# Optimization experiments

Measured on AMD Instinct MI355X. Metric: run time of the kernel, lower is better.

The kernel has to match this reference:

```python
import jax, jax.numpy as jnp
import numpy as np

N_EMBED = 1024
HEAD_SIZE = 128
B, T = 8, 2048


def setup_inputs() -> dict:
    key = jax.random.key(0)
    kx, kk, kq, kv = jax.random.split(key, 4)
    x = jax.random.normal(kx, (B, T, N_EMBED), dtype=jnp.float32)
    Wk = jax.random.normal(kk, (N_EMBED, HEAD_SIZE), dtype=jnp.float32) * (N_EMBED ** -0.5)
    Wq = jax.random.normal(kq, (N_EMBED, HEAD_SIZE), dtype=jnp.float32) * (N_EMBED ** -0.5)
    Wv = jax.random.normal(kv, (N_EMBED, HEAD_SIZE), dtype=jnp.float32) * (N_EMBED ** -0.5)
    return {"x": x, "Wk": Wk, "Wq": Wq, "Wv": Wv}


def reference(x, Wk, Wq, Wv):
    # x: [B, T, C]; single-head causal attention, dropout rate 0 (identity)
    t = x.shape[1]
    k = jnp.einsum("btc,ch->bth", x, Wk)  # keys
    q = jnp.einsum("btc,ch->bth", x, Wq)  # queries
    v = jnp.einsum("btc,ch->bth", x, Wv)  # values
    scale = k.shape[-1] ** -0.5
    scores = jnp.einsum("bqh,bkh->bqk", q, k) * scale  # [B, T, T]
    causal = jnp.tril(jnp.ones((t, t), dtype=bool))
    scores = jnp.where(causal, scores, -jnp.inf)
    attn = jax.nn.softmax(scores, axis=-1)
    return jnp.einsum("bqk,bkh->bqh", attn, v)
```

## Files before the change

### kernel.cpp

```cpp
#include <hip/hip_runtime.h>
#include <hip/hip_bf16.h>
#include <math.h>

#define B_ 8
#define T_ 2048
#define C_ 1024
#define D_ 128
#define M_ (B_*T_)

typedef __attribute__((ext_vector_type(8))) short short8;
typedef __attribute__((ext_vector_type(4))) float floatx4;
typedef __hip_bfloat16 bf16;

#define QSCALE 0.12751744416218247f

__global__ __launch_bounds__(256) void cvt_w3_kernel(const float* __restrict__ Wq,
                                                     const float* __restrict__ Wk,
                                                     const float* __restrict__ Wv,
                                                     bf16* __restrict__ Wt2) {
    __shared__ bf16 tl[64][136];
    const int t = threadIdx.x;
    const int kc = blockIdx.x, g = blockIdx.y;
    const int k0 = kc * 64;
    const float* W = (g == 0) ? Wq : (g == 1) ? Wk : Wv;
    {
        int k = t >> 2, n0 = (t & 3) * 32;
        const float* src = W + (size_t)(k0 + k) * 128 + n0;
#pragma unroll
        for (int j = 0; j < 4; ++j) {
            float4 v0 = *(const float4*)(src + j * 8);
            float4 v1 = *(const float4*)(src + j * 8 + 4);
            union { short8 s; __hip_bfloat162 h[4]; } u;
            __hip_bfloat162 h;
            h.x = __float2bfloat16(v0.x); h.y = __float2bfloat16(v0.y); u.h[0] = h;
            h.x = __float2bfloat16(v0.z); h.y = __float2bfloat16(v0.w); u.h[1] = h;
            h.x = __float2bfloat16(v1.x); h.y = __float2bfloat16(v1.y); u.h[2] = h;
            h.x = __float2bfloat16(v1.z); h.y = __float2bfloat16(v1.w); u.h[3] = h;
            *(short8*)&tl[k][n0 + j * 8] = u.s;
        }
    }
    __syncthreads();
    {
#pragma unroll
        for (int j = 0; j < 4; ++j) {
            int cid = t + j * 256;
            int lane = cid & 63, dk = (cid >> 6) & 1, cb = cid >> 7;
            int krow = dk * 32 + (lane >> 4) * 8;
            int ncol = cb * 16 + (lane & 15);
            union { short8 s; bf16 e[8]; } u;
#pragma unroll
            for (int e = 0; e < 8; ++e) u.e[e] = tl[krow + e][ncol];
            bf16* dst = Wt2 + ((((size_t)(g * 8 + cb) * 16 + kc) * 2 + dk) * 64 + lane) * 8;
            *(short8*)dst = u.s;
        }
    }
}

__global__ __launch_bounds__(256, 2) void proj11_kernel(const float* __restrict__ x,
                                                        const bf16* __restrict__ Wt2,
                                                        bf16* __restrict__ Qb,
                                                        bf16* __restrict__ Kb,
                                                        bf16* __restrict__ Vt) {
    __shared__ bf16 smem[4608];
    const int t = threadIdx.x;
    const int wave = t >> 6, lane = t & 63;
    const int quad = lane >> 4, l15 = lane & 15;
    const int row0 = blockIdx.x * 32;
    const int xrow = t >> 3, xc8 = (t & 7) * 8;
    const float* xbase = x + (size_t)(row0 + xrow) * 1024 + xc8;
    const bf16* wbase = Wt2 + (size_t)lane * 8;

    floatx4 acc[2][6];
#pragma unroll
    for (int m = 0; m < 2; ++m)
#pragma unroll
        for (int n = 0; n < 6; ++n) acc[m][n] = (floatx4)0.0f;

    float4 xr0, xr1;
    short8 br[12];

    xr0 = *(const float4*)xbase;
    xr1 = *(const float4*)(xbase + 4);
    {
        union { short8 s; __hip_bfloat162 h[4]; } u;
        __hip_bfloat162 h;
        h.x = __float2bfloat16(xr0.x); h.y = __float2bfloat16(xr0.y); u.h[0] = h;
        h.x = __float2bfloat16(xr0.z); h.y = __float2bfloat16(xr0.w); u.h[1] = h;
        h.x = __float2bfloat16(xr1.x); h.y = __float2bfloat16(xr1.y); u.h[2] = h;
        h.x = __float2bfloat16(xr1.z); h.y = __float2bfloat16(xr1.w); u.h[3] = h;
        *(short8*)&smem[xrow * 72 + xc8] = u.s;
    }
    xr0 = *(const float4*)(xbase + 64);
    xr1 = *(const float4*)(xbase + 68);
#pragma unroll
    for (int n = 0; n < 6; ++n)
#pragma unroll
        for (int dk = 0; dk < 2; ++dk)
            br[dk * 6 + n] = *(const short8*)(wbase + (size_t)(((wave * 6 + n) * 16 + 0) * 2 + dk) * 512);

    for (int kc = 0; kc < 16; ++kc) {
        __syncthreads();
        short8 brn[12];
        if (kc < 15) {
#pragma unroll
            for (int n = 0; n < 6; ++n)
#pragma unroll
                for (int dk = 0; dk < 2; ++dk)
                    brn[dk * 6 + n] = *(const short8*)(wbase + (size_t)(((wave * 6 + n) * 16 + kc + 1) * 2 + dk) * 512);
            union { short8 s; __hip_bfloat162 h[4]; } u;
            __hip_bfloat162 h;
            h.x = __float2bfloat16(xr0.x); h.y = __float2bfloat16(xr0.y); u.h[0] = h;
            h.x = __float2bfloat16(xr0.z); h.y = __float2bfloat16(xr0.w); u.h[1] = h;
            h.x = __float2bfloat16(xr1.x); h.y = __float2bfloat16(xr1.y); u.h[2] = h;
            h.x = __float2bfloat16(xr1.z); h.y = __float2bfloat16(xr1.w); u.h[3] = h;
            *(short8*)&smem[((kc + 1) & 1) * 2304 + xrow * 72 + xc8] = u.s;
        }
        if (kc < 14) {
            const float* s = xbase + (kc + 2) * 64;
            xr0 = *(const float4*)s;
            xr1 = *(const float4*)(s + 4);
        }
        const bf16* lc = smem + (kc & 1) * 2304;
#pragma unroll
        for (int dk = 0; dk < 2; ++dk) {
            short8 af[2];
#pragma unroll
            for (int m = 0; m < 2; ++m)
                af[m] = *(const short8*)&lc[(m * 16 + l15) * 72 + dk * 32 + quad * 8];
#pragma unroll
            for (int m = 0; m < 2; ++m)
#pragma unroll
                for (int n = 0; n < 6; ++n)
                    acc[m][n] = __builtin_amdgcn_mfma_f32_16x16x32_bf16(af[m], br[dk * 6 + n], acc[m][n], 0, 0, 0);
        }
        if (kc < 15) {
#pragma unroll
            for (int i = 0; i < 12; ++i) br[i] = brn[i];
        }
    }

    __syncthreads();
    bf16* vtl = smem;
#pragma unroll
    for (int m = 0; m < 2; ++m)
#pragma unroll
        for (int r = 0; r < 4; ++r) {
            const int tt = m * 16 + quad * 4 + r;
            const int row = row0 + tt;
#pragma unroll
            for (int n = 0; n < 6; ++n) {
                const int colb = wave * 96 + n * 16;
                const int g = colb >> 7;
                const int lc_ = (colb & 127) + l15;
                const float v = acc[m][n][r];
                if (g == 0)      Qb[(size_t)row * 128 + lc_] = __float2bfloat16(v * QSCALE);
                else if (g == 1) Kb[(size_t)row * 128 + lc_] = __float2bfloat16(v);
                else             vtl[tt * 137 + lc_] = __float2bfloat16(v);
            }
        }
    __syncthreads();
    {
        int d = t >> 1, toff = (t & 1) * 16;
        union { short8 s[2]; bf16 e[16]; } u;
#pragma unroll
        for (int i = 0; i < 16; ++i) u.e[i] = vtl[(toff + i) * 137 + d];
        int bb = row0 >> 11, t0 = row0 & 2047;
        bf16* dst = Vt + (size_t)(bb * D_ + d) * T_ + t0 + toff;
        *(short8*)dst       = u.s[0];
        *(short8*)(dst + 8) = u.s[1];
    }
}

__global__ __launch_bounds__(256, 3) void flash_fm2_kernel(const bf16* __restrict__ Qb,
                                                           const bf16* __restrict__ Kb,
                                                           const bf16* __restrict__ Vt,
                                                           float* __restrict__ out,
                                                           bf16* __restrict__ Opart,
                                                           float* __restrict__ Lpart) {
    const int tile = blockIdx.x, seg = blockIdx.y, b = blockIdx.z;
    const int keys_total = (tile + 1) * 64;
    const int nseg = (keys_total + 255) >> 8;
    if (seg >= nseg) return;

    __shared__ bf16 lds_k[64][136];
    __shared__ bf16 lds_v[128][72];
    __shared__ bf16 lds_p[4][16][72];
    const int t = threadIdx.x;
    const int wave = t >> 6, lane = t & 63;
    const int quad = lane >> 4, l15 = lane & 15;
    const int q0 = tile * 64;
    const int k_start = seg << 8;
    const int k_end = min(k_start + 256, keys_total);
    const int nch = (k_end - k_start) >> 6;

    short8 qf[4];
    {
        int qm = q0 + wave * 16 + l15;
#pragma unroll
        for (int dk = 0; dk < 4; ++dk)
            qf[dk] = *(const short8*)(Qb + (size_t)(b * T_ + qm) * 128 + dk * 32 + quad * 8);
    }

    short8 kreg[4], vreg[4];
    {
        const int k0 = k_start;
#pragma unroll
        for (int j = 0; j < 4; ++j) {
            int c = t + j * 256;
            { int r = c >> 4, co = (c & 15) * 8;
              kreg[j] = *(const short8*)(Kb + (size_t)(b * T_ + k0 + r) * 128 + co); }
            { int d = c >> 3, co = (c & 7) * 8;
              vreg[j] = *(const short8*)(Vt + (size_t)b * (D_ * T_) + d * T_ + k0 + co); }
        }
    }

    floatx4 o_acc[8];
#pragma unroll
    for (int i = 0; i < 8; ++i) o_acc[i] = (floatx4)0.0f;
    float lp[4] = {0.f, 0.f, 0.f, 0.f};
    const int qrow = q0 + wave * 16 + quad * 4;

    for (int ch = 0; ch < nch; ++ch) {
        const int k0 = k_start + (ch << 6);
        __syncthreads();
#pragma unroll
        for (int j = 0; j < 4; ++j) {
            int c = t + j * 256;
            { int r = c >> 4, co = (c & 15) * 8; *(short8*)&lds_k[r][co] = kreg[j]; }
            { int d = c >> 3, co = (c & 7) * 8;  *(short8*)&lds_v[d][co] = vreg[j]; }
        }
        if (ch + 1 < nch) {
            const int kn = k0 + 64;
#pragma unroll
            for (int j = 0; j < 4; ++j) {
                int c = t + j * 256;
                { int r = c >> 4, co = (c & 15) * 8;
                  kreg[j] = *(const short8*)(Kb + (size_t)(b * T_ + kn + r) * 128 + co); }
                { int d = c >> 3, co = (c & 7) * 8;
                  vreg[j] = *(const short8*)(Vt + (size_t)b * (D_ * T_) + d * T_ + kn + co); }
            }
        }
        __syncthreads();

        floatx4 s[4];
#pragma unroll
        for (int nt = 0; nt < 4; ++nt) s[nt] = (floatx4)0.0f;
#pragma unroll
        for (int dk = 0; dk < 4; ++dk)
#pragma unroll
            for (int nt = 0; nt < 4; ++nt) {
                short8 kb = *(const short8*)&lds_k[nt * 16 + l15][dk * 32 + quad * 8];
                s[nt] = __builtin_amdgcn_mfma_f32_16x16x32_bf16(qf[dk], kb, s[nt], 0, 0, 0);
            }

        float sv[4][4];
#pragma unroll
        for (int nt = 0; nt < 4; ++nt)
#pragma unroll
            for (int r = 0; r < 4; ++r) sv[nt][r] = s[nt][r];

        if (k0 + 63 > q0) {
#pragma unroll
            for (int nt = 0; nt < 4; ++nt) {
                int key = k0 + nt * 16 + l15;
#pragma unroll
                for (int r = 0; r < 4; ++r)
                    if (key > qrow + r) sv[nt][r] = -1e30f;
            }
        }

#pragma unroll
        for (int nt = 0; nt < 4; ++nt)
#pragma unroll
            for (int r = 0; r < 4; ++r) sv[nt][r] = exp2f(sv[nt][r]);
#pragma unroll
        for (int r = 0; r < 4; ++r)
            lp[r] += (sv[0][r] + sv[1][r]) + (sv[2][r] + sv[3][r]);

#pragma unroll
        for (int nt = 0; nt < 4; ++nt)
#pragma unroll
            for (int r = 0; r < 4; ++r)
                lds_p[wave][quad * 4 + r][nt * 16 + l15] = __float2bfloat16(sv[nt][r]);
        short8 pa0 = *(const short8*)&lds_p[wave][l15][quad * 8];
        short8 pa1 = *(const short8*)&lds_p[wave][l15][32 + quad * 8];

#pragma unroll
        for (int nt = 0; nt < 8; ++nt) {
            short8 vb0 = *(const short8*)&lds_v[nt * 16 + l15][quad * 8];
            short8 vb1 = *(const short8*)&lds_v[nt * 16 + l15][32 + quad * 8];
            o_acc[nt] = __builtin_amdgcn_mfma_f32_16x16x32_bf16(pa0, vb0, o_acc[nt], 0, 0, 0);
            o_acc[nt] = __builtin_amdgcn_mfma_f32_16x16x32_bf16(pa1, vb1, o_acc[nt], 0, 0, 0);
        }
    }

    float l_i[4];
#pragma unroll
    for (int r = 0; r < 4; ++r) {
        float v = lp[r];
        v += __shfl_xor(v, 1);
        v += __shfl_xor(v, 2);
        v += __shfl_xor(v, 4);
        v += __shfl_xor(v, 8);
        l_i[r] = v;
    }

    const int lrow = wave * 16 + quad * 4;
    if (nseg == 1) {
        float inv_l[4];
#pragma unroll
        for (int r = 0; r < 4; ++r) inv_l[r] = 1.0f / l_i[r];
#pragma unroll
        for (int f = 0; f < 8; ++f)
#pragma unroll
            for (int r = 0; r < 4; ++r)
                out[(size_t)(b * T_ + qrow + r) * 128 + f * 16 + l15] = o_acc[f][r] * inv_l[r];
    } else {
        int pre = 0;
        for (int u = 4; u < tile; ++u) pre += (u + 4) >> 2;
        const size_t slot = (size_t)b * 140 + pre + seg;
        bf16* ob = Opart + slot * (64 * 128);
#pragma unroll
        for (int f = 0; f < 8; ++f)
#pragma unroll
            for (int r = 0; r < 4; ++r)
                ob[(size_t)(lrow + r) * 128 + f * 16 + l15] = __float2bfloat16(o_acc[f][r]);
        if (l15 == 0) {
#pragma unroll
            for (int r = 0; r < 4; ++r)
                Lpart[slot * 64 + lrow + r] = l_i[r];
        }
    }
}

__global__ __launch_bounds__(256) void combine4_kernel(const bf16* __restrict__ Opart,
                                                       const float* __restrict__ Lpart,
                                                       float* __restrict__ out) {
    const int tile = blockIdx.x + 4, b = blockIdx.y;
    const int nseg = (tile + 4) >> 2;
    int pre = 0;
    for (int u = 4; u < tile; ++u) pre += (u + 4) >> 2;
    const size_t slot0 = (size_t)b * 140 + pre;
    const int t = threadIdx.x;
    const int row = t >> 2, c0 = (t & 3) * 32;

    float lsum = 0.f;
    for (int j = 0; j < nseg; ++j) lsum += Lpart[(slot0 + j) * 64 + row];

    float acc[32];
#pragma unroll
    for (int i = 0; i < 32; ++i) acc[i] = 0.f;
    for (int j = 0; j < nseg; ++j) {
        const bf16* src = Opart + (slot0 + j) * (64 * 128) + (size_t)row * 128 + c0;
#pragma unroll
        for (int u = 0; u < 4; ++u) {
            short8 v8 = *(const short8*)(src + u * 8);
#pragma unroll
            for (int e = 0; e < 8; ++e) {
                union { unsigned int u32; float f; } cv;
                cv.u32 = ((unsigned int)(unsigned short)v8[e]) << 16;
                acc[u * 8 + e] += cv.f;
            }
        }
    }
    float inv = 1.0f / lsum;
    float* dst = out + (size_t)(b * T_ + tile * 64 + row) * 128 + c0;
#pragma unroll
    for (int i = 0; i < 32; ++i) dst[i] = acc[i] * inv;
}

extern "C" void kernel_launch(void* const* d_in, const int* in_sizes, int n_in,
                              void* d_out, int out_size, void* d_ws, size_t ws_size,
                              hipStream_t stream) {
    const float* x  = (const float*)d_in[0];
    const float* Wk = (const float*)d_in[1];
    const float* Wq = (const float*)d_in[2];
    const float* Wv = (const float*)d_in[3];
    float* out = (float*)d_out;

    char* ws = (char*)d_ws;
    bf16*  Wt2   = (bf16*)ws;
    bf16*  Qb    = (bf16*)(ws + 786432);
    bf16*  Kb    = (bf16*)(ws + 4980736);
    bf16*  Vt    = (bf16*)(ws + 9175040);
    bf16*  Opart = (bf16*)(ws + 13369344);
    float* Lpart = (float*)(ws + 31719424);

    cvt_w3_kernel<<<dim3(16, 3), 256, 0, stream>>>(Wq, Wk, Wv, Wt2);
    proj11_kernel<<<512, 256, 0, stream>>>(x, Wt2, Qb, Kb, Vt);
    flash_fm2_kernel<<<dim3(32, 8, B_), 256, 0, stream>>>(Qb, Kb, Vt, out, Opart, Lpart);
    combine4_kernel<<<dim3(28, B_), 256, 0, stream>>>(Opart, Lpart, out);
}
```

Baseline: 82.27 us.

## Retile QKV projection to 64x192 blocks with W staged in LDS via global_load_lds

```diff
diff --git a/kernel.cpp b/kernel.cpp
--- a/kernel.cpp
+++ b/kernel.cpp
@@ -13,6 +13,10 @@
 typedef __hip_bfloat16 bf16;
 
 #define QSCALE 0.12751744416218247f
+
+#define GLDS16(gsrc, ldst) \
+    __builtin_amdgcn_global_load_lds((const __attribute__((address_space(1))) unsigned int*)(gsrc), \
+                                     (__attribute__((address_space(3))) unsigned int*)(ldst), 16, 0, 0)
 
 __global__ __launch_bounds__(256) void cvt_w3_kernel(const float* __restrict__ Wq,
                                                      const float* __restrict__ Wk,
@@ -56,19 +60,24 @@
     }
 }
 
-__global__ __launch_bounds__(256, 2) void proj11_kernel(const float* __restrict__ x,
+__global__ __launch_bounds__(256, 2) void proj12_kernel(const float* __restrict__ x,
                                                         const bf16* __restrict__ Wt2,
                                                         bf16* __restrict__ Qb,
                                                         bf16* __restrict__ Kb,
                                                         bf16* __restrict__ Vt) {
-    __shared__ bf16 smem[4608];
+    __shared__ bf16 smem[21504];
+    bf16* wlds = smem;
+    bf16* xlds = smem + 12288;
     const int t = threadIdx.x;
     const int wave = t >> 6, lane = t & 63;
     const int quad = lane >> 4, l15 = lane & 15;
-    const int row0 = blockIdx.x * 32;
-    const int xrow = t >> 3, xc8 = (t & 7) * 8;
-    const float* xbase = x + (size_t)(row0 + xrow) * 1024 + xc8;
-    const bf16* wbase = Wt2 + (size_t)lane * 8;
+    const int wr = wave >> 1, wc = wave & 1;
+    const int phys = blockIdx.x;
+    const int lb = (phys & 7) * 64 + (phys >> 3);
+    const int rt = lb >> 1, cg = lb & 1;
+    const int row0 = rt * 64;
+    const int xrow = t >> 2, xc16 = (t & 3) * 16;
+    const float* xbase = x + (size_t)(row0 + xrow) * 1024 + xc16;
 
     floatx4 acc[2][6];
 #pragma unroll
@@ -76,66 +85,65 @@
 #pragma unroll
         for (int n = 0; n < 6; ++n) acc[m][n] = (floatx4)0.0f;
 
-    float4 xr0, xr1;
-    short8 br[12];
-
-    xr0 = *(const float4*)xbase;
-    xr1 = *(const float4*)(xbase + 4);
+    float4 xf[4];
+
+#pragma unroll
+    for (int j = 0; j < 4; ++j) xf[j] = *(const float4*)(xbase + j * 4);
     {
-        union { short8 s; __hip_bfloat162 h[4]; } u;
+        union { short8 s[2]; __hip_bfloat162 h[8]; } u;
         __hip_bfloat162 h;
-        h.x = __float2bfloat16(xr0.x); h.y = __float2bfloat16(xr0.y); u.h[0] = h;
-        h.x = __float2bfloat16(xr0.z); h.y = __float2bfloat16(xr0.w); u.h[1] = h;
-        h.x = __float2bfloat16(xr1.x); h.y = __float2bfloat16(xr1.y); u.h[2] = h;
-        h.x = __float2bfloat16(xr1.z); h.y = __float2bfloat16(xr1.w); u.h[3] = h;
-        *(short8*)&smem[xrow * 72 + xc8] = u.s;
-    }
-    xr0 = *(const float4*)(xbase + 64);
-    xr1 = *(const float4*)(xbase + 68);
-#pragma unroll
-    for (int n = 0; n < 6; ++n)
-#pragma unroll
-        for (int dk = 0; dk < 2; ++dk)
-            br[dk * 6 + n] = *(const short8*)(wbase + (size_t)(((wave * 6 + n) * 16 + 0) * 2 + dk) * 512);
+#pragma unroll
+        for (int j = 0; j < 4; ++j) {
+            h.x = __float2bfloat16(xf[j].x); h.y = __float2bfloat16(xf[j].y); u.h[2 * j] = h;
+            h.x = __float2bfloat16(xf[j].z); h.y = __float2bfloat16(xf[j].w); u.h[2 * j + 1] = h;
+        }
+        *(short8*)&xlds[xrow * 72 + xc16] = u.s[0];
+        *(short8*)&xlds[xrow * 72 + xc16 + 8] = u.s[1];
+    }
+#pragma unroll
+    for (int j = 0; j < 4; ++j) xf[j] = *(const float4*)(xbase + 64 + j * 4);
 
     for (int kc = 0; kc < 16; ++kc) {
         __syncthreads();
-        short8 brn[12];
+#pragma unroll
+        for (int j = 0; j < 6; ++j) {
+            const int s = j * 4 + wave;
+            const int cbg = cg * 12 + (s >> 1);
+            const size_t chunk = ((size_t)(cbg * 16 + kc) * 2 + (s & 1));
+            GLDS16(Wt2 + chunk * 512 + lane * 8, wlds + s * 512);
+        }
         if (kc < 15) {
+            union { short8 s[2]; __hip_bfloat162 h[8]; } u;
+            __hip_bfloat162 h;
+#pragma unroll
+            for (int j = 0; j < 4; ++j) {
+                h.x = __float2bfloat16(xf[j].x); h.y = __float2bfloat16(xf[j].y); u.h[2 * j] = h;
+                h.x = __float2bfloat16(xf[j].z); h.y = __float2bfloat16(xf[j].w); u.h[2 * j + 1] = h;
+            }
+            bf16* xb = xlds + ((kc + 1) & 1) * 4608;
+            *(short8*)&xb[xrow * 72 + xc16] = u.s[0];
+            *(short8*)&xb[xrow * 72 + xc16 + 8] = u.s[1];
+        }
+        __syncthreads();
+        if (kc < 14) {
+#pragma unroll
+            for (int j = 0; j < 4; ++j) xf[j] = *(const float4*)(xbase + (kc + 2) * 64 + j * 4);
+        }
+        const bf16* xb = xlds + (kc & 1) * 4608;
+#pragma unroll
+        for (int dk = 0; dk < 2; ++dk) {
+            short8 af[2], bf[6];
+#pragma unroll
+            for (int m = 0; m < 2; ++m)
+                af[m] = *(const short8*)&xb[(wr * 32 + m * 16 + l15) * 72 + dk * 32 + quad * 8];
 #pragma unroll
             for (int n = 0; n < 6; ++n)
-#pragma unroll
-                for (int dk = 0; dk < 2; ++dk)
-                    brn[dk * 6 + n] = *(const short8*)(wbase + (size_t)(((wave * 6 + n) * 16 + kc + 1) * 2 + dk) * 512);
-            union { short8 s; __hip_bfloat162 h[4]; } u;
-            __hip_bfloat162 h;
-            h.x = __float2bfloat16(xr0.x); h.y = __float2bfloat16(xr0.y); u.h[0] = h;
-            h.x = __float2bfloat16(xr0.z); h.y = __float2bfloat16(xr0.w); u.h[1] = h;
-            h.x = __float2bfloat16(xr1.x); h.y = __float2bfloat16(xr1.y); u.h[2] = h;
-            h.x = __float2bfloat16(xr1.z); h.y = __float2bfloat16(xr1.w); u.h[3] = h;
-            *(short8*)&smem[((kc + 1) & 1) * 2304 + xrow * 72 + xc8] = u.s;
-        }
-        if (kc < 14) {
-            const float* s = xbase + (kc + 2) * 64;
-            xr0 = *(const float4*)s;
-            xr1 = *(const float4*)(s + 4);
-        }
-        const bf16* lc = smem + (kc & 1) * 2304;
-#pragma unroll
-        for (int dk = 0; dk < 2; ++dk) {
-            short8 af[2];
+                bf[n] = *(const short8*)&wlds[(size_t)((wc * 6 + n) * 2 + dk) * 512 + lane * 8];
 #pragma unroll
             for (int m = 0; m < 2; ++m)
-                af[m] = *(const short8*)&lc[(m * 16 + l15) * 72 + dk * 32 + quad * 8];
-#pragma unroll
-            for (int m = 0; m < 2; ++m)
 #pragma unroll
                 for (int n = 0; n < 6; ++n)
-                    acc[m][n] = __builtin_amdgcn_mfma_f32_16x16x32_bf16(af[m], br[dk * 6 + n], acc[m][n], 0, 0, 0);
-        }
-        if (kc < 15) {
-#pragma unroll
-            for (int i = 0; i < 12; ++i) br[i] = brn[i];
+                    acc[m][n] = __builtin_amdgcn_mfma_f32_16x16x32_bf16(af[m], bf[n], acc[m][n], 0, 0, 0);
         }
     }
 
@@ -145,29 +153,29 @@
     for (int m = 0; m < 2; ++m)
 #pragma unroll
         for (int r = 0; r < 4; ++r) {
-            const int tt = m * 16 + quad * 4 + r;
+            const int tt = wr * 32 + m * 16 + quad * 4 + r;
             const int row = row0 + tt;
 #pragma unroll
             for (int n = 0; n < 6; ++n) {
-                const int colb = wave * 96 + n * 16;
+                const int colb = cg * 192 + wc * 96 + n * 16;
                 const int g = colb >> 7;
-                const int lc_ = (colb & 127) + l15;
+                const int lc = (colb & 127) + l15;
                 const float v = acc[m][n][r];
-                if (g == 0)      Qb[(size_t)row * 128 + lc_] = __float2bfloat16(v * QSCALE);
-                else if (g == 1) Kb[(size_t)row * 128 + lc_] = __float2bfloat16(v);
-                else             vtl[tt * 137 + lc_] = __float2bfloat16(v);
-            }
-        }
-    __syncthreads();
-    {
-        int d = t >> 1, toff = (t & 1) * 16;
-        union { short8 s[2]; bf16 e[16]; } u;
-#pragma unroll
-        for (int i = 0; i < 16; ++i) u.e[i] = vtl[(toff + i) * 137 + d];
+                if (g == 0)      Qb[(size_t)row * 128 + lc] = __float2bfloat16(v * QSCALE);
+                else if (g == 1) Kb[(size_t)row * 128 + lc] = __float2bfloat16(v);
+                else             vtl[tt * 137 + lc] = __float2bfloat16(v);
+            }
+        }
+    if (cg == 1) {
+        __syncthreads();
+        int d = t >> 1, toff = (t & 1) * 32;
+        union { short8 s[4]; bf16 e[32]; } u;
+#pragma unroll
+        for (int i = 0; i < 32; ++i) u.e[i] = vtl[(toff + i) * 137 + d];
         int bb = row0 >> 11, t0 = row0 & 2047;
         bf16* dst = Vt + (size_t)(bb * D_ + d) * T_ + t0 + toff;
-        *(short8*)dst       = u.s[0];
-        *(short8*)(dst + 8) = u.s[1];
+#pragma unroll
+        for (int j = 0; j < 4; ++j) *(short8*)(dst + j * 8) = u.s[j];
     }
 }
 
@@ -387,7 +395,7 @@
     float* Lpart = (float*)(ws + 31719424);
 
     cvt_w3_kernel<<<dim3(16, 3), 256, 0, stream>>>(Wq, Wk, Wv, Wt2);
-    proj11_kernel<<<512, 256, 0, stream>>>(x, Wt2, Qb, Kb, Vt);
+    proj12_kernel<<<512, 256, 0, stream>>>(x, Wt2, Qb, Kb, Vt);
     flash_fm2_kernel<<<dim3(32, 8, B_), 256, 0, stream>>>(Qb, Kb, Vt, out, Opart, Lpart);
     combine4_kernel<<<dim3(28, B_), 256, 0, stream>>>(Opart, Lpart, out);
 }
```

After: 86.08 us. +4.6%, slower.
